# Kernel optimization log

Measured on AMD Instinct MI355X. Metric: run time of the kernel, lower is better.

## Reference

```python
import jax, jax.numpy as jnp
import numpy as np

B, T, D, H = 64, 1024, 512, 512

def setup_inputs() -> dict:
    key = jax.random.key(0)
    k1, k2, k3, k4 = jax.random.split(key, 4)
    x = jax.random.normal(k1, (B, T, D), dtype=jnp.float32)
    # Keras LSTM weights: kernel [D, 4H], recurrent_kernel [H, 4H], bias [4H]
    # gate order: i, f, c(g), o
    kernel = jax.random.normal(k2, (D, 4 * H), dtype=jnp.float32) * 0.05
    recurrent_kernel = jax.random.normal(k3, (H, 4 * H), dtype=jnp.float32) * 0.05
    bias = jax.random.normal(k4, (4 * H,), dtype=jnp.float32) * 0.05
    return {"x": x, "kernel": kernel, "recurrent_kernel": recurrent_kernel, "bias": bias}

def reference(x, kernel, recurrent_kernel, bias):
    # Precompute input projections for all timesteps: [B, T, 4H]
    xW = jnp.einsum('btd,dg->btg', x, kernel) + bias
    xW_t = jnp.transpose(xW, (1, 0, 2))  # [T, B, 4H] for scan over time
    h0 = jnp.zeros((x.shape[0], recurrent_kernel.shape[0]), dtype=x.dtype)
    c0 = jnp.zeros_like(h0)

    def step(carry, xw):
        h, c = carry
        z = xw + h @ recurrent_kernel  # [B, 4H]
        i, f, g, o = jnp.split(z, 4, axis=-1)
        i = jax.nn.sigmoid(i)
        f = jax.nn.sigmoid(f)
        g = jnp.tanh(g)
        o = jax.nn.sigmoid(o)
        c_new = f * c + i * g
        h_new = o * jnp.tanh(c_new)
        return (h_new, c_new), None

    (h_final, _), _ = jax.lax.scan(step, (h0, c0), xW_t)
    return h_final  # [B, H]
```

## Files before the change

kernel.cpp:

```cpp
#include <hip/hip_runtime.h>


#define B_  64
#define T_  1024
#define D_  512
#define H_  512
#define G4H 2048

typedef _Float16 half8 __attribute__((ext_vector_type(8)));
typedef _Float16 half4 __attribute__((ext_vector_type(4)));
typedef float    f32x4 __attribute__((ext_vector_type(4)));
typedef unsigned long long ull;
typedef unsigned int u32;

static __device__ __forceinline__ float sigm(float x) { return 1.f / (1.f + __expf(-x)); }
static __device__ __forceinline__ float tanh_(float x) {
    float xc = fminf(fmaxf(x, -15.f), 15.f);
    float e  = __expf(2.f * xc);
    return (e - 1.f) / (e + 1.f);
}
static __device__ __forceinline__ float lo16f(unsigned u) {
    return (float)__builtin_bit_cast(_Float16, (unsigned short)(u & 0xffffu));
}
static __device__ __forceinline__ float hi16f(unsigned u) {
    return (float)__builtin_bit_cast(_Float16, (unsigned short)(u >> 16));
}
static __device__ __forceinline__ void gload_lds16(const _Float16* g, _Float16* l) {
    __builtin_amdgcn_global_load_lds((const __attribute__((address_space(1))) u32*)g,
                                     (__attribute__((address_space(3))) u32*)l, 16, 0, 0);
}

__global__ void trans_w(const float* __restrict__ W, _Float16* __restrict__ WT) {
    int idx = blockIdx.x * blockDim.x + threadIdx.x;
    int total = D_ * G4H;
    int stride = gridDim.x * blockDim.x;
    for (int i = idx; i < total; i += stride) {
        int k = i >> 11;
        int n = i & (G4H - 1);
        WT[(size_t)n * D_ + k] = (_Float16)W[i];
    }
}

__global__ void conv_x(const float* __restrict__ x, _Float16* __restrict__ xh) {
    int idx = blockIdx.x * blockDim.x + threadIdx.x;
    int total = (B_ * T_ * D_) / 4;
    int stride = gridDim.x * blockDim.x;
    const f32x4* xi = (const f32x4*)x;
    half4* xo = (half4*)xh;
    for (int i = idx; i < total; i += stride) {
        f32x4 v = xi[i];
        xo[i] = (half4){(_Float16)v.x, (_Float16)v.y, (_Float16)v.z, (_Float16)v.w};
    }
}

__global__ void zero_buf(unsigned* __restrict__ p, int n) {
    int idx = blockIdx.x * blockDim.x + threadIdx.x;
    int stride = gridDim.x * blockDim.x;
    for (int i = idx; i < n; i += stride) p[i] = 0u;
}

__global__ __launch_bounds__(256) void gemm_xw_f16(const _Float16* __restrict__ xh,
                                                   const _Float16* __restrict__ WkT,
                                                   const float* __restrict__ bias,
                                                   _Float16* __restrict__ xw, int tbase) {
    __shared__ _Float16 As[128 * 64];
    __shared__ _Float16 Bs[128 * 64];
    const int tid  = threadIdx.x;
    const int lane = tid & 63;
    const int wave = tid >> 6;
    const int l15  = lane & 15;
    const int quad = lane >> 4;
    const int b     = blockIdx.z;
    const int n0    = blockIdx.x * 128;
    const int tloc0 = blockIdx.y * 128;

    const int srow = tid >> 3;
    const int sseg = tid & 7;

    f32x4 acc[2][8];
#pragma unroll
    for (int rt = 0; rt < 2; ++rt)
#pragma unroll
        for (int ct = 0; ct < 8; ++ct) acc[rt][ct] = (f32x4){0.f, 0.f, 0.f, 0.f};

    const _Float16* abase = xh + ((size_t)b * T_ + tbase + tloc0) * D_;
    const _Float16* bbase = WkT + (size_t)n0 * D_;

    for (int kb = 0; kb < 8; ++kb) {
        __syncthreads();
#pragma unroll
        for (int q = 0; q < 4; ++q) {
            int row  = q * 32 + srow;
            int col2 = (sseg * 16) ^ ((row & 7) << 4);
            _Float16* ldst = (_Float16*)((char*)As + q * 4096 + wave * 1024);
            gload_lds16(abase + (size_t)row * D_ + kb * 64 + (col2 >> 1), ldst);
            _Float16* ldstb = (_Float16*)((char*)Bs + q * 4096 + wave * 1024);
            gload_lds16(bbase + (size_t)row * D_ + kb * 64 + (col2 >> 1), ldstb);
        }
        __syncthreads();
#pragma unroll
        for (int ks = 0; ks < 2; ++ks) {
            half8 af[2];
#pragma unroll
            for (int rt = 0; rt < 2; ++rt) {
                int row = wave * 32 + rt * 16 + l15;
                int c2  = (ks * 64 + quad * 16) ^ ((row & 7) << 4);
                af[rt] = *(const half8*)&As[row * 64 + (c2 >> 1)];
            }
#pragma unroll
            for (int ct = 0; ct < 8; ++ct) {
                int brw = ct * 16 + l15;
                int c2  = (ks * 64 + quad * 16) ^ ((brw & 7) << 4);
                half8 bf = *(const half8*)&Bs[brw * 64 + (c2 >> 1)];
                acc[0][ct] = __builtin_amdgcn_mfma_f32_16x16x32_f16(af[0], bf, acc[0][ct], 0, 0, 0);
                acc[1][ct] = __builtin_amdgcn_mfma_f32_16x16x32_f16(af[1], bf, acc[1][ct], 0, 0, 0);
            }
        }
    }
#pragma unroll
    for (int ct = 0; ct < 8; ++ct) {
        int col = n0 + ct * 16 + l15;
        float bs = bias[col];
#pragma unroll
        for (int rt = 0; rt < 2; ++rt)
#pragma unroll
            for (int r = 0; r < 4; ++r) {
                int tt = tloc0 + wave * 32 + rt * 16 + quad * 4 + r;
                xw[((size_t)tt * B_ + b) * G4H + col] = (_Float16)(acc[rt][ct][r] + bs);
            }
    }
}

__global__ __launch_bounds__(256) void gemm_xw_small(const float* __restrict__ x,
                                                     const _Float16* __restrict__ WkT,
                                                     const float* __restrict__ bias,
                                                     _Float16* __restrict__ xw,
                                                     int tbase) {
    __shared__ _Float16 As[64][40];
    __shared__ _Float16 Bst[64][40];
    const int tid  = threadIdx.x;
    const int lane = tid & 63;
    const int wave = tid >> 6;
    const int l15  = lane & 15;
    const int quad = lane >> 4;
    const int b     = blockIdx.z;
    const int n0    = blockIdx.x * 64;
    const int tloc0 = blockIdx.y * 64;

    const float* xbase = x + ((size_t)b * T_ + (tbase + tloc0)) * D_;
    f32x4 acc[4];
#pragma unroll
    for (int i = 0; i < 4; ++i) acc[i] = (f32x4){0.f, 0.f, 0.f, 0.f};

    const int ai = tid >> 2, ac = tid & 3;
    const int bn = tid >> 2, bq = tid & 3;

    for (int kb = 0; kb < 16; ++kb) {
        __syncthreads();
        const float* ap = xbase + (size_t)ai * D_ + kb * 32 + ac * 8;
        f32x4 av0 = *(const f32x4*)ap;
        f32x4 av1 = *(const f32x4*)(ap + 4);
        half8 ah = { (_Float16)av0.x, (_Float16)av0.y, (_Float16)av0.z, (_Float16)av0.w,
                     (_Float16)av1.x, (_Float16)av1.y, (_Float16)av1.z, (_Float16)av1.w };
        *(half8*)&As[ai][ac * 8] = ah;
        half8 bv = *(const half8*)(WkT + (size_t)(n0 + bn) * D_ + kb * 32 + bq * 8);
        *(half8*)&Bst[bn][bq * 8] = bv;
        __syncthreads();

        half8 afrag = *(const half8*)&As[16 * wave + l15][quad * 8];
#pragma unroll
        for (int nt = 0; nt < 4; ++nt) {
            half8 bfrag = *(const half8*)&Bst[nt * 16 + l15][quad * 8];
            acc[nt] = __builtin_amdgcn_mfma_f32_16x16x32_f16(afrag, bfrag, acc[nt], 0, 0, 0);
        }
    }
#pragma unroll
    for (int nt = 0; nt < 4; ++nt)
#pragma unroll
        for (int r = 0; r < 4; ++r) {
            int tt  = tloc0 + 16 * wave + quad * 4 + r;
            int col = n0 + nt * 16 + l15;
            xw[((size_t)tt * B_ + b) * G4H + col] = (_Float16)(acc[nt][r] + bias[col]);
        }
}

__global__ __launch_bounds__(256, 1) void lstm_scan(const _Float16* __restrict__ xw,
                                                    const _Float16* __restrict__ WrT,
                                                    unsigned* __restrict__ hbuf,
                                                    float* __restrict__ cio,
                                                    float* __restrict__ out,
                                                    int t0, int t1) {
    const int w    = blockIdx.x;
    const int g    = w & 3;
    const int s    = w >> 2;
    const int u0   = s * 32;
    const int tid  = threadIdx.x;
    const int lane = tid & 63;
    const int wave = tid >> 6;
    const int l15  = lane & 15;
    const int quad = lane >> 4;

    half8 bfrag[2][16];
#pragma unroll
    for (int ct = 0; ct < 2; ++ct) {
        const int col = wave * H_ + u0 + ct * 16 + l15;
        const _Float16* wp = WrT + (size_t)col * D_;
#pragma unroll
        for (int kt = 0; kt < 16; ++kt)
            bfrag[ct][kt] = *(const half8*)(wp + kt * 32 + quad * 8);
    }

    const int rho  = tid >> 4;
    const int jj   = tid & 15;
    const int brow = g * 16 + rho;
    const int un0  = u0 + 2 * jj;
    float c0 = 0.f, c1 = 0.f;
    if (t0 != 0) {
        c0 = cio[(size_t)brow * H_ + un0];
        c1 = cio[(size_t)brow * H_ + un0 + 1];
    }

    __shared__ _Float16 hS[16][520];
    __shared__ float    zS[16][4][34];

    const size_t slotSz = (size_t)B_ * H_;

    for (int t = t0; t < t1; ++t) {
        const unsigned* xwd = (const unsigned*)(xw + ((size_t)(t - t0) * B_ + brow) * G4H);
        const int dbase = (u0 >> 1) + jj;
        unsigned xwi = xwd[0 * 256 + dbase];
        unsigned xwf = xwd[1 * 256 + dbase];
        unsigned xwg = xwd[2 * 256 + dbase];
        unsigned xwo = xwd[3 * 256 + dbase];

        if (t > 0) {
            const ull* src = (const ull*)(hbuf + (size_t)((t - 1) % 3) * slotSz)
                             + (size_t)(g * 16) * 256 + tid;
            const unsigned tgt = (unsigned)(t & 0xffff);
            const ull expect = ((ull)tgt << 16) | ((ull)tgt << 48);
            ull v[16];
            int guard = 0;
            while (true) {
                ull diff = 0;
#pragma unroll
                for (int k = 0; k < 16; ++k)
                    v[k] = __hip_atomic_load(src + (size_t)k * 256,
                                             __ATOMIC_RELAXED, __HIP_MEMORY_SCOPE_AGENT);
#pragma unroll
                for (int k = 0; k < 16; ++k)
                    diff |= (v[k] ^ expect) & 0xffff0000ffff0000ull;
                if (diff == 0) break;
                if (++guard > 8192) break;
            }
#pragma unroll
            for (int k = 0; k < 16; ++k) {
                unsigned p = (unsigned)(v[k] & 0xffffu) | (((unsigned)(v[k] >> 32)) << 16);
                *(unsigned*)&hS[k][2 * tid] = p;
            }
        }
        __syncthreads();

        f32x4 a0 = {0.f,0.f,0.f,0.f}, a1 = a0, b0 = a0, b1 = a0;
        if (t > 0) {
#pragma unroll
            for (int kt = 0; kt < 16; kt += 2) {
                half8 af0 = *(const half8*)&hS[l15][kt * 32 + quad * 8];
                half8 af1 = *(const half8*)&hS[l15][(kt + 1) * 32 + quad * 8];
                a0 = __builtin_amdgcn_mfma_f32_16x16x32_f16(af0, bfrag[0][kt],     a0, 0, 0, 0);
                a1 = __builtin_amdgcn_mfma_f32_16x16x32_f16(af0, bfrag[1][kt],     a1, 0, 0, 0);
                b0 = __builtin_amdgcn_mfma_f32_16x16x32_f16(af1, bfrag[0][kt + 1], b0, 0, 0, 0);
                b1 = __builtin_amdgcn_mfma_f32_16x16x32_f16(af1, bfrag[1][kt + 1], b1, 0, 0, 0);
            }
        }
        f32x4 z0 = a0 + b0, z1 = a1 + b1;
#pragma unroll
        for (int r = 0; r < 4; ++r) {
            zS[quad * 4 + r][wave][l15]      = z0[r];
            zS[quad * 4 + r][wave][16 + l15] = z1[r];
        }
        __syncthreads();

        float zi0 = zS[rho][0][2*jj] + lo16f(xwi), zi1 = zS[rho][0][2*jj+1] + hi16f(xwi);
        float zf0 = zS[rho][1][2*jj] + lo16f(xwf), zf1 = zS[rho][1][2*jj+1] + hi16f(xwf);
        float zg0 = zS[rho][2][2*jj] + lo16f(xwg), zg1 = zS[rho][2][2*jj+1] + hi16f(xwg);
        float zo0 = zS[rho][3][2*jj] + lo16f(xwo), zo1 = zS[rho][3][2*jj+1] + hi16f(xwo);

        c0 = sigm(zf0) * c0 + sigm(zi0) * tanh_(zg0);
        c1 = sigm(zf1) * c1 + sigm(zi1) * tanh_(zg1);
        float h0 = sigm(zo0) * tanh_(c0);
        float h1 = sigm(zo1) * tanh_(c1);

        const unsigned tagw = ((unsigned)((t + 1) & 0xffff)) << 16;
        unsigned d0 = (unsigned)__builtin_bit_cast(unsigned short, (_Float16)h0) | tagw;
        unsigned d1 = (unsigned)__builtin_bit_cast(unsigned short, (_Float16)h1) | tagw;
        ull wv = (ull)d0 | ((ull)d1 << 32);
        __hip_atomic_store((ull*)(hbuf + (size_t)(t % 3) * slotSz) + (size_t)brow * 256 + (un0 >> 1),
                           wv, __ATOMIC_RELAXED, __HIP_MEMORY_SCOPE_AGENT);

        if (t == T_ - 1) {
            out[(size_t)brow * H_ + un0]     = h0;
            out[(size_t)brow * H_ + un0 + 1] = h1;
        }
    }
    cio[(size_t)brow * H_ + un0]     = c0;
    cio[(size_t)brow * H_ + un0 + 1] = c1;
}

extern "C" void kernel_launch(void* const* d_in, const int* in_sizes, int n_in,
                              void* d_out, int out_size, void* d_ws, size_t ws_size,
                              hipStream_t stream) {
    (void)in_sizes; (void)n_in;
    const float* x    = (const float*)d_in[0];
    const float* Wk   = (const float*)d_in[1];
    const float* Wr   = (const float*)d_in[2];
    const float* bias = (const float*)d_in[3];
    float* out = (float*)d_out;

    char* ws = (char*)d_ws;
    _Float16* WkT  = (_Float16*)(ws + 1024);
    _Float16* WrT  = (_Float16*)(ws + 1024 + 2097152);
    unsigned* hbuf = (unsigned*)(ws + 1024 + 2 * 2097152);
    float*    cio  = (float*)(ws + 1024 + 2 * 2097152 + 393216);
    const size_t fixed   = 1024 + 2 * 2097152 + 393216 + 131072;
    const size_t xhBytes = (size_t)B_ * T_ * D_ * 2;
    const size_t perT    = (size_t)B_ * G4H * 2;

    size_t avail = (ws_size > fixed) ? ws_size - fixed : 0;
    bool use_xh = avail >= xhBytes + 128 * perT;
    _Float16* xh = (_Float16*)(ws + fixed);
    _Float16* xw = (_Float16*)(ws + fixed + (use_xh ? xhBytes : 0));

    int ct = 0;
    if (use_xh) {
        const int cands[4] = {1024, 512, 256, 128};
        size_t av2 = avail - xhBytes;
        for (int i = 0; i < 4; ++i)
            if ((size_t)cands[i] * perT <= av2) { ct = cands[i]; break; }
    } else {
        const int cands[5] = {1024, 512, 256, 128, 64};
        for (int i = 0; i < 5; ++i)
            if ((size_t)cands[i] * perT <= avail) { ct = cands[i]; break; }
    }
    if (ct == 0) {
        hipMemsetAsync(d_out, 0, (size_t)out_size * 4, stream);
        return;
    }

    zero_buf<<<96, 256, 0, stream>>>(hbuf, 3 * B_ * H_);
    trans_w<<<512, 256, 0, stream>>>(Wk, WkT);
    trans_w<<<512, 256, 0, stream>>>(Wr, WrT);
    if (use_xh) conv_x<<<2048, 256, 0, stream>>>(x, xh);

    for (int t0 = 0; t0 < T_; t0 += ct) {
        if (use_xh)
            gemm_xw_f16<<<dim3(16, ct / 128, B_), 256, 0, stream>>>(xh, WkT, bias, xw, t0);
        else
            gemm_xw_small<<<dim3(32, ct / 64, B_), 256, 0, stream>>>(x, WkT, bias, xw, t0);
        lstm_scan<<<64, 256, 0, stream>>>(xw, WrT, hbuf, cio, out, t0, t0 + ct);
    }
}
```

Before: 3.167 ms.

## Fuse input-projection GEMM and LSTM scan into one producer/consumer persistent kernel

A single kernel now runs the input-projection GEMM and the recurrent scan together. 64 blocks run the recurrence and 192 producer blocks compute xW tiles in chunks of 128 timesteps, signalling completion through atomic counters. The scan blocks spin on the counter for each chunk before consuming it. This overlaps the GEMM with the serial recurrence instead of running them back to back. The price is co-residency assumptions, a spin-wait with a guard, and contention between producers and the latency-critical scan blocks.

```diff
diff --git a/kernel.cpp b/kernel.cpp
--- a/kernel.cpp
+++ b/kernel.cpp
@@ -6,6 +6,9 @@
 #define D_  512
 #define H_  512
 #define G4H 2048
+#define NPROD 192
+#define TILES_TOTAL 8192
+#define TILES_PER_CHUNK 1024
 
 typedef _Float16 half8 __attribute__((ext_vector_type(8)));
 typedef _Float16 half4 __attribute__((ext_vector_type(4)));
@@ -59,75 +62,207 @@
     for (int i = idx; i < n; i += stride) p[i] = 0u;
 }
 
-__global__ __launch_bounds__(256) void gemm_xw_f16(const _Float16* __restrict__ xh,
-                                                   const _Float16* __restrict__ WkT,
-                                                   const float* __restrict__ bias,
-                                                   _Float16* __restrict__ xw, int tbase) {
+__global__ __launch_bounds__(256, 1) void lstm_fused(const _Float16* __restrict__ xh,
+                                                     const _Float16* __restrict__ WkT,
+                                                     const float* __restrict__ bias,
+                                                     _Float16* __restrict__ xw,
+                                                     const _Float16* __restrict__ WrT,
+                                                     unsigned* __restrict__ hbuf,
+                                                     float* __restrict__ out,
+                                                     unsigned* __restrict__ ctrl) {
     __shared__ _Float16 As[128 * 64];
     __shared__ _Float16 Bs[128 * 64];
+    __shared__ _Float16 hS[16][520];
+    __shared__ float    zS[16][4][34];
+
     const int tid  = threadIdx.x;
     const int lane = tid & 63;
     const int wave = tid >> 6;
     const int l15  = lane & 15;
     const int quad = lane >> 4;
-    const int b     = blockIdx.z;
-    const int n0    = blockIdx.x * 128;
-    const int tloc0 = blockIdx.y * 128;
-
-    const int srow = tid >> 3;
-    const int sseg = tid & 7;
-
-    f32x4 acc[2][8];
-#pragma unroll
-    for (int rt = 0; rt < 2; ++rt)
-#pragma unroll
-        for (int ct = 0; ct < 8; ++ct) acc[rt][ct] = (f32x4){0.f, 0.f, 0.f, 0.f};
-
-    const _Float16* abase = xh + ((size_t)b * T_ + tbase + tloc0) * D_;
-    const _Float16* bbase = WkT + (size_t)n0 * D_;
-
-    for (int kb = 0; kb < 8; ++kb) {
-        __syncthreads();
-#pragma unroll
-        for (int q = 0; q < 4; ++q) {
-            int row  = q * 32 + srow;
-            int col2 = (sseg * 16) ^ ((row & 7) << 4);
-            _Float16* ldst = (_Float16*)((char*)As + q * 4096 + wave * 1024);
-            gload_lds16(abase + (size_t)row * D_ + kb * 64 + (col2 >> 1), ldst);
-            _Float16* ldstb = (_Float16*)((char*)Bs + q * 4096 + wave * 1024);
-            gload_lds16(bbase + (size_t)row * D_ + kb * 64 + (col2 >> 1), ldstb);
-        }
-        __syncthreads();
-#pragma unroll
-        for (int ks = 0; ks < 2; ++ks) {
-            half8 af[2];
-#pragma unroll
-            for (int rt = 0; rt < 2; ++rt) {
-                int row = wave * 32 + rt * 16 + l15;
-                int c2  = (ks * 64 + quad * 16) ^ ((row & 7) << 4);
-                af[rt] = *(const half8*)&As[row * 64 + (c2 >> 1)];
+
+    if (blockIdx.x >= 64) {
+        const int p = blockIdx.x - 64;
+        const int srow = tid >> 3;
+        const int sseg = tid & 7;
+        for (int tau = p; tau < TILES_TOTAL; tau += NPROD) {
+            const int chunk = tau >> 10;
+            const int loc   = tau & 1023;
+            const int n0    = (loc & 15) * 128;
+            const int b     = loc >> 4;
+            const int tb    = chunk * 128;
+
+            f32x4 acc[2][8];
+#pragma unroll
+            for (int rt = 0; rt < 2; ++rt)
+#pragma unroll
+                for (int ct = 0; ct < 8; ++ct) acc[rt][ct] = (f32x4){0.f, 0.f, 0.f, 0.f};
+
+            const _Float16* abase = xh + ((size_t)b * T_ + tb) * D_;
+            const _Float16* bbase = WkT + (size_t)n0 * D_;
+
+            for (int kb = 0; kb < 8; ++kb) {
+                __syncthreads();
+#pragma unroll
+                for (int q = 0; q < 4; ++q) {
+                    int row  = q * 32 + srow;
+                    int col2 = (sseg * 16) ^ ((row & 7) << 4);
+                    _Float16* ldst = (_Float16*)((char*)As + q * 4096 + wave * 1024);
+                    gload_lds16(abase + (size_t)row * D_ + kb * 64 + (col2 >> 1), ldst);
+                    _Float16* ldstb = (_Float16*)((char*)Bs + q * 4096 + wave * 1024);
+                    gload_lds16(bbase + (size_t)row * D_ + kb * 64 + (col2 >> 1), ldstb);
+                }
+                __syncthreads();
+#pragma unroll
+                for (int ks = 0; ks < 2; ++ks) {
+                    half8 af[2];
+#pragma unroll
+                    for (int rt = 0; rt < 2; ++rt) {
+                        int row = wave * 32 + rt * 16 + l15;
+                        int c2  = (ks * 64 + quad * 16) ^ ((row & 7) << 4);
+                        af[rt] = *(const half8*)&As[row * 64 + (c2 >> 1)];
+                    }
+#pragma unroll
+                    for (int ct = 0; ct < 8; ++ct) {
+                        int brw = ct * 16 + l15;
+                        int c2  = (ks * 64 + quad * 16) ^ ((brw & 7) << 4);
+                        half8 bf = *(const half8*)&Bs[brw * 64 + (c2 >> 1)];
+                        acc[0][ct] = __builtin_amdgcn_mfma_f32_16x16x32_f16(af[0], bf, acc[0][ct], 0, 0, 0);
+                        acc[1][ct] = __builtin_amdgcn_mfma_f32_16x16x32_f16(af[1], bf, acc[1][ct], 0, 0, 0);
+                    }
+                }
             }
 #pragma unroll
             for (int ct = 0; ct < 8; ++ct) {
-                int brw = ct * 16 + l15;
-                int c2  = (ks * 64 + quad * 16) ^ ((brw & 7) << 4);
-                half8 bf = *(const half8*)&Bs[brw * 64 + (c2 >> 1)];
-                acc[0][ct] = __builtin_amdgcn_mfma_f32_16x16x32_f16(af[0], bf, acc[0][ct], 0, 0, 0);
-                acc[1][ct] = __builtin_amdgcn_mfma_f32_16x16x32_f16(af[1], bf, acc[1][ct], 0, 0, 0);
-            }
-        }
-    }
-#pragma unroll
-    for (int ct = 0; ct < 8; ++ct) {
-        int col = n0 + ct * 16 + l15;
-        float bs = bias[col];
-#pragma unroll
-        for (int rt = 0; rt < 2; ++rt)
-#pragma unroll
-            for (int r = 0; r < 4; ++r) {
-                int tt = tloc0 + wave * 32 + rt * 16 + quad * 4 + r;
-                xw[((size_t)tt * B_ + b) * G4H + col] = (_Float16)(acc[rt][ct][r] + bs);
-            }
+                int col = n0 + ct * 16 + l15;
+                float bs = bias[col];
+#pragma unroll
+                for (int rt = 0; rt < 2; ++rt)
+#pragma unroll
+                    for (int r = 0; r < 4; ++r) {
+                        int tt = tb + wave * 32 + rt * 16 + quad * 4 + r;
+                        xw[((size_t)tt * B_ + b) * G4H + col] = (_Float16)(acc[rt][ct][r] + bs);
+                    }
+            }
+            __syncthreads();
+            if (tid == 0)
+                __hip_atomic_fetch_add(&ctrl[16 + 16 * chunk], 1u,
+                                       __ATOMIC_RELEASE, __HIP_MEMORY_SCOPE_AGENT);
+        }
+        return;
+    }
+
+    const int w    = blockIdx.x;
+    const int g    = w & 3;
+    const int s    = w >> 2;
+    const int u0   = s * 32;
+    const int gt   = wave;
+
+    half8 bfrag[2][16];
+#pragma unroll
+    for (int ct = 0; ct < 2; ++ct) {
+        const int col = gt * H_ + u0 + ct * 16 + l15;
+        const _Float16* wp = WrT + (size_t)col * D_;
+#pragma unroll
+        for (int kt = 0; kt < 16; ++kt)
+            bfrag[ct][kt] = *(const half8*)(wp + kt * 32 + quad * 8);
+    }
+
+    const int rho  = tid >> 4;
+    const int jj   = tid & 15;
+    const int brow = g * 16 + rho;
+    const int un0  = u0 + 2 * jj;
+    float c0 = 0.f, c1 = 0.f;
+
+    const size_t slotSz = (size_t)B_ * H_;
+
+    for (int t = 0; t < T_; ++t) {
+        if ((t & 127) == 0) {
+            if (tid == 0) {
+                int gd = 0;
+                while (__hip_atomic_load(&ctrl[16 + 16 * (t >> 7)], __ATOMIC_RELAXED,
+                                         __HIP_MEMORY_SCOPE_AGENT) < TILES_PER_CHUNK
+                       && ++gd < (1 << 20)) {}
+            }
+            __syncthreads();
+            __builtin_amdgcn_fence(__ATOMIC_ACQUIRE, "agent");
+        }
+
+        const unsigned* xwd = (const unsigned*)(xw + ((size_t)t * B_ + brow) * G4H);
+        const int dbase = (u0 >> 1) + jj;
+        unsigned xwi = xwd[0 * 256 + dbase];
+        unsigned xwf = xwd[1 * 256 + dbase];
+        unsigned xwg = xwd[2 * 256 + dbase];
+        unsigned xwo = xwd[3 * 256 + dbase];
+
+        if (t > 0) {
+            const ull* src = (const ull*)(hbuf + (size_t)((t - 1) % 3) * slotSz)
+                             + (size_t)(g * 16) * 256 + tid;
+            const unsigned tgt = (unsigned)(t & 0xffff);
+            const ull expect = ((ull)tgt << 16) | ((ull)tgt << 48);
+            ull v[16];
+            int guard = 0;
+            while (true) {
+                ull diff = 0;
+#pragma unroll
+                for (int k = 0; k < 16; ++k)
+                    v[k] = __hip_atomic_load(src + (size_t)k * 256,
+                                             __ATOMIC_RELAXED, __HIP_MEMORY_SCOPE_AGENT);
+#pragma unroll
+                for (int k = 0; k < 16; ++k)
+                    diff |= (v[k] ^ expect) & 0xffff0000ffff0000ull;
+                if (diff == 0) break;
+                if (++guard > 8192) break;
+            }
+#pragma unroll
+            for (int k = 0; k < 16; ++k) {
+                unsigned pk = (unsigned)(v[k] & 0xffffu) | (((unsigned)(v[k] >> 32)) << 16);
+                *(unsigned*)&hS[k][2 * tid] = pk;
+            }
+        }
+        __syncthreads();
+
+        f32x4 a0 = {0.f,0.f,0.f,0.f}, a1 = a0, b0 = a0, b1 = a0;
+        if (t > 0) {
+#pragma unroll
+            for (int kt = 0; kt < 16; kt += 2) {
+                half8 af0 = *(const half8*)&hS[l15][kt * 32 + quad * 8];
+                half8 af1 = *(const half8*)&hS[l15][(kt + 1) * 32 + quad * 8];
+                a0 = __builtin_amdgcn_mfma_f32_16x16x32_f16(af0, bfrag[0][kt],     a0, 0, 0, 0);
+                a1 = __builtin_amdgcn_mfma_f32_16x16x32_f16(af0, bfrag[1][kt],     a1, 0, 0, 0);
+                b0 = __builtin_amdgcn_mfma_f32_16x16x32_f16(af1, bfrag[0][kt + 1], b0, 0, 0, 0);
+                b1 = __builtin_amdgcn_mfma_f32_16x16x32_f16(af1, bfrag[1][kt + 1], b1, 0, 0, 0);
+            }
+        }
+        f32x4 z0 = a0 + b0, z1 = a1 + b1;
+#pragma unroll
+        for (int r = 0; r < 4; ++r) {
+            zS[quad * 4 + r][gt][l15]      = z0[r];
+            zS[quad * 4 + r][gt][16 + l15] = z1[r];
+        }
+        __syncthreads();
+
+        float zi0 = zS[rho][0][2*jj] + lo16f(xwi), zi1 = zS[rho][0][2*jj+1] + hi16f(xwi);
+        float zf0 = zS[rho][1][2*jj] + lo16f(xwf), zf1 = zS[rho][1][2*jj+1] + hi16f(xwf);
+        float zg0 = zS[rho][2][2*jj] + lo16f(xwg), zg1 = zS[rho][2][2*jj+1] + hi16f(xwg);
+        float zo0 = zS[rho][3][2*jj] + lo16f(xwo), zo1 = zS[rho][3][2*jj+1] + hi16f(xwo);
+
+        c0 = sigm(zf0) * c0 + sigm(zi0) * tanh_(zg0);
+        c1 = sigm(zf1) * c1 + sigm(zi1) * tanh_(zg1);
+        float h0 = sigm(zo0) * tanh_(c0);
+        float h1 = sigm(zo1) * tanh_(c1);
+
+        const unsigned tagw = ((unsigned)((t + 1) & 0xffff)) << 16;
+        unsigned d0 = (unsigned)__builtin_bit_cast(unsigned short, (_Float16)h0) | tagw;
+        unsigned d1 = (unsigned)__builtin_bit_cast(unsigned short, (_Float16)h1) | tagw;
+        ull wv = (ull)d0 | ((ull)d1 << 32);
+        __hip_atomic_store((ull*)(hbuf + (size_t)(t % 3) * slotSz) + (size_t)brow * 256 + (un0 >> 1),
+                           wv, __ATOMIC_RELAXED, __HIP_MEMORY_SCOPE_AGENT);
+
+        if (t == T_ - 1) {
+            out[(size_t)brow * H_ + un0]     = h0;
+            out[(size_t)brow * H_ + un0 + 1] = h1;
+        }
     }
 }
 
@@ -151,7 +286,6 @@
     f32x4 acc[4];
 #pragma unroll
     for (int i = 0; i < 4; ++i) acc[i] = (f32x4){0.f, 0.f, 0.f, 0.f};
-
     const int ai = tid >> 2, ac = tid & 3;
     const int bn = tid >> 2, bq = tid & 3;
 
@@ -222,7 +356,6 @@
 
     __shared__ _Float16 hS[16][520];
     __shared__ float    zS[16][4][34];
-
     const size_t slotSz = (size_t)B_ * H_;
 
     for (int t = t0; t < t1; ++t) {
@@ -321,41 +454,39 @@
     _Float16* WrT  = (_Float16*)(ws + 1024 + 2097152);
     unsigned* hbuf = (unsigned*)(ws + 1024 + 2 * 2097152);
     float*    cio  = (float*)(ws + 1024 + 2 * 2097152 + 393216);
+    unsigned* ctrl = (unsigned*)cio;
     const size_t fixed   = 1024 + 2 * 2097152 + 393216 + 131072;
     const size_t xhBytes = (size_t)B_ * T_ * D_ * 2;
     const size_t perT    = (size_t)B_ * G4H * 2;
 
     size_t avail = (ws_size > fixed) ? ws_size - fixed : 0;
-    bool use_xh = avail >= xhBytes + 128 * perT;
     _Float16* xh = (_Float16*)(ws + fixed);
-    _Float16* xw = (_Float16*)(ws + fixed + (use_xh ? xhBytes : 0));
-
+    bool fused_ok = avail >= xhBytes + (size_t)T_ * perT;
+
+    if (fused_ok) {
+        _Float16* xw = (_Float16*)(ws + fixed + xhBytes);
+        zero_buf<<<96, 256, 0, stream>>>(hbuf, 3 * B_ * H_ + 256);
+        trans_w<<<512, 256, 0, stream>>>(Wk, WkT);
+        trans_w<<<512, 256, 0, stream>>>(Wr, WrT);
+        conv_x<<<2048, 256, 0, stream>>>(x, xh);
+        lstm_fused<<<64 + NPROD, 256, 0, stream>>>(xh, WkT, bias, xw, WrT, hbuf, out, ctrl);
+        return;
+    }
+
+    _Float16* xw = (_Float16*)(ws + fixed);
     int ct = 0;
-    if (use_xh) {
-        const int cands[4] = {1024, 512, 256, 128};
-        size_t av2 = avail - xhBytes;
-        for (int i = 0; i < 4; ++i)
-            if ((size_t)cands[i] * perT <= av2) { ct = cands[i]; break; }
-    } else {
-        const int cands[5] = {1024, 512, 256, 128, 64};
-        for (int i = 0; i < 5; ++i)
-            if ((size_t)cands[i] * perT <= avail) { ct = cands[i]; break; }
-    }
+    const int cands[5] = {1024, 512, 256, 128, 64};
+    for (int i = 0; i < 5; ++i)
+        if ((size_t)cands[i] * perT <= avail) { ct = cands[i]; break; }
     if (ct == 0) {
         hipMemsetAsync(d_out, 0, (size_t)out_size * 4, stream);
         return;
     }
-
     zero_buf<<<96, 256, 0, stream>>>(hbuf, 3 * B_ * H_);
     trans_w<<<512, 256, 0, stream>>>(Wk, WkT);
     trans_w<<<512, 256, 0, stream>>>(Wr, WrT);
-    if (use_xh) conv_x<<<2048, 256, 0, stream>>>(x, xh);
-
     for (int t0 = 0; t0 < T_; t0 += ct) {
-        if (use_xh)
-            gemm_xw_f16<<<dim3(16, ct / 128, B_), 256, 0, stream>>>(xh, WkT, bias, xw, t0);
-        else
-            gemm_xw_small<<<dim3(32, ct / 64, B_), 256, 0, stream>>>(x, WkT, bias, xw, t0);
+        gemm_xw_small<<<dim3(32, ct / 64, B_), 256, 0, stream>>>(x, WkT, bias, xw, t0);
         lstm_scan<<<64, 256, 0, stream>>>(xw, WrT, hbuf, cio, out, t0, t0 + ct);
     }
 }
```

Measured after the change: 3.276 ms. +3.5%, slower.
